# Optimization experiments

Measured on AMD Instinct MI355X. Metric: run time of the kernel, lower is better.

Reference implementation:

```python
import jax, jax.numpy as jnp
import numpy as np

N_ITEMS = 100000
N_EDGES = 800000
D = 64
N_LAYERS = 3  # config['ii_layers']


def setup_inputs() -> dict:
    key = jax.random.key(0)
    k1, k2, k3, k4 = jax.random.split(key, 4)
    rows = jax.random.randint(k1, (N_EDGES,), 0, N_ITEMS, dtype=jnp.int64 if jax.config.jax_enable_x64 else jnp.int32)
    cols = jax.random.randint(k2, (N_EDGES,), 0, N_ITEMS, dtype=jnp.int64 if jax.config.jax_enable_x64 else jnp.int32)
    vals = jax.random.uniform(k3, (N_EDGES,), dtype=jnp.float32)
    item_embeddings = jax.random.normal(k4, (N_ITEMS, D), dtype=jnp.float32)
    return {"rows": rows, "cols": cols, "vals": vals, "item_embeddings": item_embeddings}


def _spmm(rows, cols, vals, x):
    # sparse.mm(A, x) with A in COO: out[r] += vals[e] * x[c] for each edge e=(r,c)
    msgs = vals[:, None] * x[cols]            # [E, D] gathered & weighted messages
    return jax.ops.segment_sum(msgs, rows, num_segments=N_ITEMS)


def reference(rows, cols, vals, item_embeddings):
    # HyperConv: iterate SpMM, average initial + all layer outputs (fused running sum).
    acc = item_embeddings
    cur = item_embeddings
    for _ in range(N_LAYERS):
        cur = _spmm(rows, cols, vals, cur)
        acc = acc + cur
    return acc / jnp.asarray(N_LAYERS + 1, dtype=item_embeddings.dtype)
```

## Files before the change

### kernel.cpp

```cpp
#include <hip/hip_runtime.h>
#include <hip/hip_fp16.h>


#define NI 100000
#define NE 800000
#define DD 64

#define RPB  512
#define BINS ((NI + RPB - 1) / RPB)
#define EPB  4096
#define P1B  ((NE + EPB - 1) / EPB)
#define CAP  5120
#define BC   32

__global__ __launch_bounds__(256) void part1_k(const int* __restrict__ rows,
                                               const int* __restrict__ cols,
                                               const float* __restrict__ vals,
                                               int* __restrict__ bin_cnt,
                                               int2* __restrict__ binned) {
    __shared__ int hist[BINS], base[BINS], cur[BINS];
    int t = threadIdx.x;
    for (int i = t; i < BINS; i += 256) hist[i] = 0;
    __syncthreads();
    int e0 = blockIdx.x * EPB;
    for (int i = t; i < EPB; i += 256) {
        int e = e0 + i;
        if (e < NE) atomicAdd(&hist[rows[e] >> 9], 1);
    }
    __syncthreads();
    for (int i = t; i < BINS; i += 256) {
        int c = hist[i];
        base[i] = c ? atomicAdd(&bin_cnt[i], c) : 0;
        cur[i] = 0;
    }
    __syncthreads();
    for (int i = t; i < EPB; i += 256) {
        int e = e0 + i;
        if (e < NE) {
            int r = rows[e];
            int b = r >> 9;
            int pos = base[b] + atomicAdd(&cur[b], 1);
            if (pos < CAP)
                binned[(size_t)b * CAP + pos] =
                    make_int2(((r & 511) << 17) | cols[e], __float_as_int(vals[e]));
        }
    }
}

__global__ __launch_bounds__(256) void part2_k(const int* __restrict__ bin_cnt,
                                               const int2* __restrict__ binned,
                                               int2* __restrict__ bucket,
                                               int* __restrict__ fill) {
    __shared__ int cur[RPB];
    int t = threadIdx.x;
    int b = blockIdx.x;
    for (int i = t; i < RPB; i += 256) cur[i] = 0;
    __syncthreads();
    int cnt = bin_cnt[b];
    if (cnt > CAP) cnt = CAP;
    const int2* src = binned + (size_t)b * CAP;
    for (int i = t; i < cnt; i += 256) {
        int2 e = src[i];
        int rl = e.x >> 17;
        int pos = atomicAdd(&cur[rl], 1);
        if (pos < BC)
            bucket[((size_t)b * RPB + rl) * BC + pos] = make_int2(e.x & 0x1FFFF, e.y);
    }
    __syncthreads();
    for (int i = t; i < RPB; i += 256) {
        int r = b * RPB + i;
        if (r < NI) {
            int c = (cur[i] < BC) ? cur[i] : BC;
            if (c & 1) {
                bucket[((size_t)b * RPB + i) * BC + c] = make_int2(0, 0);
                c++;
            }
            fill[r] = c;
        }
    }
}

__global__ __launch_bounds__(256) void convert_k(const float4* __restrict__ x,
                                                 __half* __restrict__ xh, int n4) {
    int i = blockIdx.x * 256 + threadIdx.x;
    if (i < n4) {
        float4 v = x[i];
        __half2* dst = (__half2*)(xh + (size_t)i * 4);
        dst[0] = __floats2half2_rn(v.x, v.y);
        dst[1] = __floats2half2_rn(v.z, v.w);
    }
}

template <int MODE>
__global__ __launch_bounds__(256) void spmm_k(const int* __restrict__ fill,
                                              const int2* __restrict__ bucket,
                                              const __half* __restrict__ xin,
                                              __half* __restrict__ nxt,
                                              const float* __restrict__ x0,
                                              const __half* __restrict__ s1,
                                              float* __restrict__ outp) {
    int tid  = threadIdx.x;
    int lane = tid & 63;
    int grp  = lane >> 3;
    int ll   = lane & 7;
    int r    = blockIdx.x * 32 + (tid >> 6) * 8 + grp;
    int deg  = fill[r];
    const int2* ep = bucket + (size_t)r * BC;

    float a0 = 0.f, a1 = 0.f, a2 = 0.f, a3 = 0.f;
    float a4 = 0.f, a5 = 0.f, a6 = 0.f, a7 = 0.f;

    for (int j = 0; j < deg; j += 2) {
        int2 e0 = ep[j];
        int2 e1 = ep[j + 1];
        const uint4* p0 = (const uint4*)(xin + (size_t)e0.x * DD + 8 * ll);
        const uint4* p1 = (const uint4*)(xin + (size_t)e1.x * DD + 8 * ll);
        uint4 g0 = *p0;
        uint4 g1 = *p1;
        float v0 = __int_as_float(e0.y);
        float v1 = __int_as_float(e1.y);
        float2 f;
        f = __half22float2(*(__half2*)&g0.x); a0 += v0 * f.x; a1 += v0 * f.y;
        f = __half22float2(*(__half2*)&g0.y); a2 += v0 * f.x; a3 += v0 * f.y;
        f = __half22float2(*(__half2*)&g0.z); a4 += v0 * f.x; a5 += v0 * f.y;
        f = __half22float2(*(__half2*)&g0.w); a6 += v0 * f.x; a7 += v0 * f.y;
        f = __half22float2(*(__half2*)&g1.x); a0 += v1 * f.x; a1 += v1 * f.y;
        f = __half22float2(*(__half2*)&g1.y); a2 += v1 * f.x; a3 += v1 * f.y;
        f = __half22float2(*(__half2*)&g1.z); a4 += v1 * f.x; a5 += v1 * f.y;
        f = __half22float2(*(__half2*)&g1.w); a6 += v1 * f.x; a7 += v1 * f.y;
    }

    if (MODE == 2) {
        size_t fo = (size_t)r * DD + 8 * ll;
        const float4* xp = (const float4*)(x0 + fo);
        float4 xa = xp[0], xb = xp[1];
        uint4 s1u = *(const uint4*)(s1 + fo);
        uint4 s2u = *(const uint4*)(xin + fo);
        float4 oa, ob;
        float2 f1, f2;
        f1 = __half22float2(*(__half2*)&s1u.x); f2 = __half22float2(*(__half2*)&s2u.x);
        oa.x = (xa.x + f1.x + f2.x + a0) * 0.25f;
        oa.y = (xa.y + f1.y + f2.y + a1) * 0.25f;
        f1 = __half22float2(*(__half2*)&s1u.y); f2 = __half22float2(*(__half2*)&s2u.y);
        oa.z = (xa.z + f1.x + f2.x + a2) * 0.25f;
        oa.w = (xa.w + f1.y + f2.y + a3) * 0.25f;
        f1 = __half22float2(*(__half2*)&s1u.z); f2 = __half22float2(*(__half2*)&s2u.z);
        ob.x = (xb.x + f1.x + f2.x + a4) * 0.25f;
        ob.y = (xb.y + f1.y + f2.y + a5) * 0.25f;
        f1 = __half22float2(*(__half2*)&s1u.w); f2 = __half22float2(*(__half2*)&s2u.w);
        ob.z = (xb.z + f1.x + f2.x + a6) * 0.25f;
        ob.w = (xb.w + f1.y + f2.y + a7) * 0.25f;
        float4* op = (float4*)(outp + fo);
        op[0] = oa;
        op[1] = ob;
    } else {
        uint4 o;
        __half2 h;
        h = __floats2half2_rn(a0, a1); o.x = *(uint*)&h;
        h = __floats2half2_rn(a2, a3); o.y = *(uint*)&h;
        h = __floats2half2_rn(a4, a5); o.z = *(uint*)&h;
        h = __floats2half2_rn(a6, a7); o.w = *(uint*)&h;
        *(uint4*)(nxt + (size_t)r * DD + 8 * ll) = o;
    }
}

#define NB ((NI + 255) / 256)

__global__ __launch_bounds__(256) void init_k(const float4* __restrict__ x,
                                              float4* __restrict__ cur,
                                              float4* __restrict__ acc, int n4) {
    int i = blockIdx.x * 256 + threadIdx.x;
    if (i < n4) { float4 v = x[i]; cur[i] = v; acc[i] = v; }
}

__global__ __launch_bounds__(256) void hist_k(const int* __restrict__ rows,
                                              int* __restrict__ counts) {
    int e = blockIdx.x * 256 + threadIdx.x;
    if (e < NE) atomicAdd(&counts[rows[e]], 1);
}

__global__ __launch_bounds__(256) void scan1_k(const int* __restrict__ counts,
                                               int* __restrict__ bsum) {
    __shared__ int s[256];
    int t = threadIdx.x;
    int i = blockIdx.x * 256 + t;
    s[t] = (i < NI) ? counts[i] : 0;
    __syncthreads();
    for (int off = 128; off > 0; off >>= 1) {
        if (t < off) s[t] += s[t + off];
        __syncthreads();
    }
    if (t == 0) bsum[blockIdx.x] = s[0];
}

__global__ __launch_bounds__(512) void scan2_k(int* __restrict__ bsum) {
    __shared__ int s[512];
    int t = threadIdx.x;
    int v = (t < NB) ? bsum[t] : 0;
    s[t] = v;
    __syncthreads();
    for (int off = 1; off < 512; off <<= 1) {
        int tmp = (t >= off) ? s[t - off] : 0;
        __syncthreads();
        s[t] += tmp;
        __syncthreads();
    }
    if (t < NB) bsum[t] = s[t] - v;
}

__global__ __launch_bounds__(256) void scan3_k(const int* __restrict__ counts,
                                               const int* __restrict__ bsum,
                                               int* __restrict__ rowptr) {
    __shared__ int s[256];
    int t = threadIdx.x;
    int i = blockIdx.x * 256 + t;
    int v = (i < NI) ? counts[i] : 0;
    s[t] = v;
    __syncthreads();
    for (int off = 1; off < 256; off <<= 1) {
        int tmp = (t >= off) ? s[t - off] : 0;
        __syncthreads();
        s[t] += tmp;
        __syncthreads();
    }
    int excl = s[t] - v + bsum[blockIdx.x];
    if (i < NI) rowptr[i] = excl;
    if (i == NI - 1) rowptr[NI] = excl + v;
}

__global__ __launch_bounds__(256) void scatter_k(const int* __restrict__ rows,
                                                 const int* __restrict__ cols,
                                                 const float* __restrict__ vals,
                                                 const int* __restrict__ rowptr,
                                                 int* __restrict__ fillc,
                                                 int2* __restrict__ edges) {
    int e = blockIdx.x * 256 + threadIdx.x;
    if (e < NE) {
        int r = rows[e];
        int pos = rowptr[r] + atomicAdd(&fillc[r], 1);
        edges[pos] = make_int2(cols[e], __float_as_int(vals[e]));
    }
}

__global__ __launch_bounds__(256) void spmm_csr_k(const int* __restrict__ rowptr,
                                                  const int2* __restrict__ edges,
                                                  const float* __restrict__ x,
                                                  float* __restrict__ nxt,
                                                  float* __restrict__ acc,
                                                  int last) {
    int r = __builtin_amdgcn_readfirstlane(blockIdx.x * 4 + (threadIdx.x >> 6));
    int lane = threadIdx.x & 63;
    int beg = rowptr[r];
    int end = rowptr[r + 1];
    float s = 0.f;
    int j = beg;
    for (; j + 3 < end; j += 4) {
        int2 e0 = edges[j], e1 = edges[j + 1], e2 = edges[j + 2], e3 = edges[j + 3];
        float g0 = x[(size_t)e0.x * DD + lane];
        float g1 = x[(size_t)e1.x * DD + lane];
        float g2 = x[(size_t)e2.x * DD + lane];
        float g3 = x[(size_t)e3.x * DD + lane];
        s += __int_as_float(e0.y) * g0; s += __int_as_float(e1.y) * g1;
        s += __int_as_float(e2.y) * g2; s += __int_as_float(e3.y) * g3;
    }
    for (; j < end; ++j) {
        int2 e = edges[j];
        s += __int_as_float(e.y) * x[(size_t)e.x * DD + lane];
    }
    size_t o = (size_t)r * DD + lane;
    if (last) acc[o] = (acc[o] + s) * 0.25f;
    else { nxt[o] = s; acc[o] += s; }
}

extern "C" void kernel_launch(void* const* d_in, const int* in_sizes, int n_in,
                              void* d_out, int out_size, void* d_ws, size_t ws_size,
                              hipStream_t stream) {
    const int*   rows = (const int*)d_in[0];
    const int*   cols = (const int*)d_in[1];
    const float* vals = (const float*)d_in[2];
    const float* x    = (const float*)d_in[3];
    float* outp = (float*)d_out;

    const size_t fbuf  = (size_t)NI * DD * sizeof(float);
    const size_t hbuf  = (size_t)NI * DD * sizeof(__half);
    const int    n4        = NI * DD / 4;
    const int    grid_elem = (n4 + 255) / 256;

    char* wsp = (char*)d_ws;

    size_t off_xh     = 0;
    size_t off_s1     = off_xh + hbuf;
    size_t off_s2     = off_s1 + hbuf;
    size_t off_bucket = off_s2 + hbuf;
    size_t off_binned = off_bucket + (size_t)NI * BC * 8;
    size_t off_fill   = off_binned + (size_t)BINS * CAP * 8;
    size_t off_bcnt   = off_fill + (size_t)NI * 4;
    size_t need       = off_bcnt + (size_t)BINS * 4;

    if (ws_size >= need) {
        __half* xh      = (__half*)(wsp + off_xh);
        __half* s1h     = (__half*)(wsp + off_s1);
        __half* s2h     = (__half*)(wsp + off_s2);
        int2*   bucket  = (int2*)(wsp + off_bucket);
        int2*   binned  = (int2*)(wsp + off_binned);
        int*    fill    = (int*)(wsp + off_fill);
        int*    bin_cnt = (int*)(wsp + off_bcnt);

        hipMemsetAsync(bin_cnt, 0, BINS * sizeof(int), stream);
        part1_k<<<P1B, 256, 0, stream>>>(rows, cols, vals, bin_cnt, binned);
        part2_k<<<BINS, 256, 0, stream>>>(bin_cnt, binned, bucket, fill);
        convert_k<<<grid_elem, 256, 0, stream>>>((const float4*)x, xh, n4);

        const int grid_spmm = NI / 32;
        spmm_k<0><<<grid_spmm, 256, 0, stream>>>(fill, bucket, xh,  s1h, nullptr, nullptr, nullptr);
        spmm_k<1><<<grid_spmm, 256, 0, stream>>>(fill, bucket, s1h, s2h, nullptr, nullptr, nullptr);
        spmm_k<2><<<grid_spmm, 256, 0, stream>>>(fill, bucket, s2h, nullptr, x, s1h, outp);
        return;
    }

    const int grid_edge = (NE + 255) / 256;
    const int grid_csr  = NI / 4;

    float* bufA   = (float*)wsp;
    float* bufB   = (float*)(wsp + fbuf);
    int2*  edges  = (int2*)(wsp + 2 * fbuf);
    int*   rowptr = (int*)(wsp + 2 * fbuf + (size_t)NE * 8);
    int*   counts = rowptr + (NI + 1);
    int*   bsum   = counts + NI;

    hipMemsetAsync(counts, 0, NI * sizeof(int), stream);
    hist_k<<<grid_edge, 256, 0, stream>>>(rows, counts);
    scan1_k<<<NB, 256, 0, stream>>>(counts, bsum);
    scan2_k<<<1, 512, 0, stream>>>(bsum);
    scan3_k<<<NB, 256, 0, stream>>>(counts, bsum, rowptr);
    hipMemsetAsync(counts, 0, NI * sizeof(int), stream);
    scatter_k<<<grid_edge, 256, 0, stream>>>(rows, cols, vals, rowptr, counts, edges);
    init_k<<<grid_elem, 256, 0, stream>>>((const float4*)x, (float4*)bufA,
                                          (float4*)outp, n4);
    spmm_csr_k<<<grid_csr, 256, 0, stream>>>(rowptr, edges, bufA, bufB, outp, 0);
    spmm_csr_k<<<grid_csr, 256, 0, stream>>>(rowptr, edges, bufB, bufA, outp, 0);
    spmm_csr_k<<<grid_csr, 256, 0, stream>>>(rowptr, edges, bufA, bufB, outp, 1);
}
```

Measured before the change: 188.4 us.

## Replace capped per-row buckets with exact CSR and chunk-major feature layout

Measured after the change: 495.5 us. 163% more time.

```diff
diff --git a/kernel.cpp b/kernel.cpp
--- a/kernel.cpp
+++ b/kernel.cpp
@@ -5,13 +5,14 @@
 #define NI 100000
 #define NE 800000
 #define DD 64
+#define NCH 8
+#define CF  8
 
 #define RPB  512
 #define BINS ((NI + RPB - 1) / RPB)
-#define EPB  4096
+#define EPB  1024
 #define P1B  ((NE + EPB - 1) / EPB)
 #define CAP  5120
-#define BC   32
 
 __global__ __launch_bounds__(256) void part1_k(const int* __restrict__ rows,
                                                const int* __restrict__ cols,
@@ -49,93 +50,120 @@
 
 __global__ __launch_bounds__(256) void part2_k(const int* __restrict__ bin_cnt,
                                                const int2* __restrict__ binned,
-                                               int2* __restrict__ bucket,
-                                               int* __restrict__ fill) {
-    __shared__ int cur[RPB];
+                                               int2* __restrict__ edges,
+                                               int* __restrict__ rowptr) {
+    __shared__ int cur[RPB], off[RPB];
+    __shared__ long long ecache[CAP];
+    __shared__ int bb;
     int t = threadIdx.x;
     int b = blockIdx.x;
+
     for (int i = t; i < RPB; i += 256) cur[i] = 0;
-    __syncthreads();
-    int cnt = bin_cnt[b];
-    if (cnt > CAP) cnt = CAP;
+    if (t < BINS) off[t] = min(bin_cnt[t], CAP);
+    __syncthreads();
+    if (t == 0) {
+        int s = 0;
+        for (int i = 0; i < b; i++) s += off[i];
+        bb = s;
+    }
+    int cnt = min(bin_cnt[b], CAP);
     const int2* src = binned + (size_t)b * CAP;
+    __syncthreads();
     for (int i = t; i < cnt; i += 256) {
         int2 e = src[i];
-        int rl = e.x >> 17;
-        int pos = atomicAdd(&cur[rl], 1);
-        if (pos < BC)
-            bucket[((size_t)b * RPB + rl) * BC + pos] = make_int2(e.x & 0x1FFFF, e.y);
+        atomicAdd(&cur[e.x >> 17], 1);
+        ecache[i] = ((long long)e.y << 32) | (unsigned int)e.x;
+    }
+    __syncthreads();
+    if (t < 64) {
+        int base_i = t * 8;
+        int loc[8];
+        int s = 0;
+        #pragma unroll
+        for (int k = 0; k < 8; k++) { loc[k] = s; s += cur[base_i + k]; }
+        int excl = s;
+        #pragma unroll
+        for (int d = 1; d < 64; d <<= 1) {
+            int v = __shfl_up(excl, d, 64);
+            if (t >= d) excl += v;
+        }
+        excl -= s;
+        #pragma unroll
+        for (int k = 0; k < 8; k++) off[base_i + k] = excl + loc[k];
     }
     __syncthreads();
     for (int i = t; i < RPB; i += 256) {
         int r = b * RPB + i;
-        if (r < NI) {
-            int c = (cur[i] < BC) ? cur[i] : BC;
-            if (c & 1) {
-                bucket[((size_t)b * RPB + i) * BC + c] = make_int2(0, 0);
-                c++;
-            }
-            fill[r] = c;
-        }
-    }
-}
-
-__global__ __launch_bounds__(256) void convert_k(const float4* __restrict__ x,
-                                                 __half* __restrict__ xh, int n4) {
-    int i = blockIdx.x * 256 + threadIdx.x;
-    if (i < n4) {
-        float4 v = x[i];
-        __half2* dst = (__half2*)(xh + (size_t)i * 4);
-        dst[0] = __floats2half2_rn(v.x, v.y);
-        dst[1] = __floats2half2_rn(v.z, v.w);
+        if (r < NI) rowptr[r] = bb + off[i];
+        cur[i] = 0;
+    }
+    if (b == BINS - 1 && t == 0) rowptr[NI] = bb + cnt;
+    __syncthreads();
+    for (int i = t; i < cnt; i += 256) {
+        long long e = ecache[i];
+        int lo = (int)e;
+        int rl = (lo >> 17) & 511;
+        int pos = bb + off[rl] + atomicAdd(&cur[rl], 1);
+        edges[pos] = make_int2(lo & 0x1FFFF, (int)(e >> 32));
+    }
+}
+
+__global__ __launch_bounds__(256) void convert_k(const float* __restrict__ x,
+                                                 __half* __restrict__ xh) {
+    int r = blockIdx.x * 256 + threadIdx.x;
+    int c = blockIdx.y;
+    if (r < NI) {
+        const float4* xp = (const float4*)(x + (size_t)r * DD + c * CF);
+        float4 xa = xp[0], xb = xp[1];
+        uint4 o;
+        __half2 h;
+        h = __floats2half2_rn(xa.x, xa.y); o.x = *(unsigned int*)&h;
+        h = __floats2half2_rn(xa.z, xa.w); o.y = *(unsigned int*)&h;
+        h = __floats2half2_rn(xb.x, xb.y); o.z = *(unsigned int*)&h;
+        h = __floats2half2_rn(xb.w, xb.w); o.w = *(unsigned int*)&h;
+        h = __floats2half2_rn(xb.z, xb.w); o.w = *(unsigned int*)&h;
+        *(uint4*)(xh + (size_t)c * NI * CF + (size_t)r * CF) = o;
     }
 }
 
 template <int MODE>
-__global__ __launch_bounds__(256) void spmm_k(const int* __restrict__ fill,
-                                              const int2* __restrict__ bucket,
+__global__ __launch_bounds__(256) void spmm_k(const int* __restrict__ rowptr,
+                                              const long long* __restrict__ edges,
                                               const __half* __restrict__ xin,
                                               __half* __restrict__ nxt,
                                               const float* __restrict__ x0,
                                               const __half* __restrict__ s1,
                                               float* __restrict__ outp) {
-    int tid  = threadIdx.x;
-    int lane = tid & 63;
-    int grp  = lane >> 3;
-    int ll   = lane & 7;
-    int r    = blockIdx.x * 32 + (tid >> 6) * 8 + grp;
-    int deg  = fill[r];
-    const int2* ep = bucket + (size_t)r * BC;
+    int chunk  = blockIdx.x & 7;
+    int rowblk = blockIdx.x >> 3;
+    int r = rowblk * 256 + threadIdx.x;
+    bool act = (r < NI);
+    int beg = act ? rowptr[r] : 0;
+    int end = act ? rowptr[r + 1] : 0;
+    const __half* xc = xin + (size_t)chunk * NI * CF;
 
     float a0 = 0.f, a1 = 0.f, a2 = 0.f, a3 = 0.f;
     float a4 = 0.f, a5 = 0.f, a6 = 0.f, a7 = 0.f;
 
-    for (int j = 0; j < deg; j += 2) {
-        int2 e0 = ep[j];
-        int2 e1 = ep[j + 1];
-        const uint4* p0 = (const uint4*)(xin + (size_t)e0.x * DD + 8 * ll);
-        const uint4* p1 = (const uint4*)(xin + (size_t)e1.x * DD + 8 * ll);
-        uint4 g0 = *p0;
-        uint4 g1 = *p1;
-        float v0 = __int_as_float(e0.y);
-        float v1 = __int_as_float(e1.y);
+    for (int j = beg; j < end; ++j) {
+        long long e = __builtin_nontemporal_load(edges + j);
+        int col = (int)e;
+        float v = __int_as_float((int)(e >> 32));
+        uint4 g = *(const uint4*)(xc + (size_t)col * CF);
         float2 f;
-        f = __half22float2(*(__half2*)&g0.x); a0 += v0 * f.x; a1 += v0 * f.y;
-        f = __half22float2(*(__half2*)&g0.y); a2 += v0 * f.x; a3 += v0 * f.y;
-        f = __half22float2(*(__half2*)&g0.z); a4 += v0 * f.x; a5 += v0 * f.y;
-        f = __half22float2(*(__half2*)&g0.w); a6 += v0 * f.x; a7 += v0 * f.y;
-        f = __half22float2(*(__half2*)&g1.x); a0 += v1 * f.x; a1 += v1 * f.y;
-        f = __half22float2(*(__half2*)&g1.y); a2 += v1 * f.x; a3 += v1 * f.y;
-        f = __half22float2(*(__half2*)&g1.z); a4 += v1 * f.x; a5 += v1 * f.y;
-        f = __half22float2(*(__half2*)&g1.w); a6 += v1 * f.x; a7 += v1 * f.y;
-    }
-
+        f = __half22float2(*(__half2*)&g.x); a0 += v * f.x; a1 += v * f.y;
+        f = __half22float2(*(__half2*)&g.y); a2 += v * f.x; a3 += v * f.y;
+        f = __half22float2(*(__half2*)&g.z); a4 += v * f.x; a5 += v * f.y;
+        f = __half22float2(*(__half2*)&g.w); a6 += v * f.x; a7 += v * f.y;
+    }
+
+    if (!act) return;
+    size_t co = (size_t)chunk * NI * CF + (size_t)r * CF;
     if (MODE == 2) {
-        size_t fo = (size_t)r * DD + 8 * ll;
-        const float4* xp = (const float4*)(x0 + fo);
+        const float4* xp = (const float4*)(x0 + (size_t)r * DD + chunk * CF);
         float4 xa = xp[0], xb = xp[1];
-        uint4 s1u = *(const uint4*)(s1 + fo);
-        uint4 s2u = *(const uint4*)(xin + fo);
+        uint4 s1u = *(const uint4*)(s1 + co);
+        uint4 s2u = *(const uint4*)(xin + co);
         float4 oa, ob;
         float2 f1, f2;
         f1 = __half22float2(*(__half2*)&s1u.x); f2 = __half22float2(*(__half2*)&s2u.x);
@@ -150,17 +178,17 @@
         f1 = __half22float2(*(__half2*)&s1u.w); f2 = __half22float2(*(__half2*)&s2u.w);
         ob.z = (xb.z + f1.x + f2.x + a6) * 0.25f;
         ob.w = (xb.w + f1.y + f2.y + a7) * 0.25f;
-        float4* op = (float4*)(outp + fo);
+        float4* op = (float4*)(outp + (size_t)r * DD + chunk * CF);
         op[0] = oa;
         op[1] = ob;
     } else {
         uint4 o;
         __half2 h;
-        h = __floats2half2_rn(a0, a1); o.x = *(uint*)&h;
-        h = __floats2half2_rn(a2, a3); o.y = *(uint*)&h;
-        h = __floats2half2_rn(a4, a5); o.z = *(uint*)&h;
-        h = __floats2half2_rn(a6, a7); o.w = *(uint*)&h;
-        *(uint4*)(nxt + (size_t)r * DD + 8 * ll) = o;
+        h = __floats2half2_rn(a0, a1); o.x = *(unsigned int*)&h;
+        h = __floats2half2_rn(a2, a3); o.y = *(unsigned int*)&h;
+        h = __floats2half2_rn(a4, a5); o.z = *(unsigned int*)&h;
+        h = __floats2half2_rn(a6, a7); o.w = *(unsigned int*)&h;
+        *(uint4*)(nxt + co) = o;
     }
 }
 
@@ -281,49 +309,52 @@
     const float* x    = (const float*)d_in[3];
     float* outp = (float*)d_out;
 
-    const size_t fbuf  = (size_t)NI * DD * sizeof(float);
-    const size_t hbuf  = (size_t)NI * DD * sizeof(__half);
-    const int    n4        = NI * DD / 4;
-    const int    grid_elem = (n4 + 255) / 256;
+    const size_t fbuf = (size_t)NI * DD * sizeof(float);
+    const size_t hbuf = (size_t)NI * DD * sizeof(__half);
 
     char* wsp = (char*)d_ws;
 
     size_t off_xh     = 0;
     size_t off_s1     = off_xh + hbuf;
     size_t off_s2     = off_s1 + hbuf;
-    size_t off_bucket = off_s2 + hbuf;
-    size_t off_binned = off_bucket + (size_t)NI * BC * 8;
-    size_t off_fill   = off_binned + (size_t)BINS * CAP * 8;
-    size_t off_bcnt   = off_fill + (size_t)NI * 4;
+    size_t off_binned = off_s2 + hbuf;
+    size_t off_edges  = off_binned + (size_t)BINS * CAP * 8;
+    size_t off_rowptr = off_edges + (size_t)NE * 8;
+    size_t off_bcnt   = off_rowptr + ((size_t)NI + 2) * 4;
     size_t need       = off_bcnt + (size_t)BINS * 4;
 
     if (ws_size >= need) {
         __half* xh      = (__half*)(wsp + off_xh);
         __half* s1h     = (__half*)(wsp + off_s1);
         __half* s2h     = (__half*)(wsp + off_s2);
-        int2*   bucket  = (int2*)(wsp + off_bucket);
         int2*   binned  = (int2*)(wsp + off_binned);
-        int*    fill    = (int*)(wsp + off_fill);
+        int2*   edges   = (int2*)(wsp + off_edges);
+        int*    rowptr  = (int*)(wsp + off_rowptr);
         int*    bin_cnt = (int*)(wsp + off_bcnt);
 
         hipMemsetAsync(bin_cnt, 0, BINS * sizeof(int), stream);
         part1_k<<<P1B, 256, 0, stream>>>(rows, cols, vals, bin_cnt, binned);
-        part2_k<<<BINS, 256, 0, stream>>>(bin_cnt, binned, bucket, fill);
-        convert_k<<<grid_elem, 256, 0, stream>>>((const float4*)x, xh, n4);
-
-        const int grid_spmm = NI / 32;
-        spmm_k<0><<<grid_spmm, 256, 0, stream>>>(fill, bucket, xh,  s1h, nullptr, nullptr, nullptr);
-        spmm_k<1><<<grid_spmm, 256, 0, stream>>>(fill, bucket, s1h, s2h, nullptr, nullptr, nullptr);
-        spmm_k<2><<<grid_spmm, 256, 0, stream>>>(fill, bucket, s2h, nullptr, x, s1h, outp);
+        part2_k<<<BINS, 256, 0, stream>>>(bin_cnt, binned, edges, rowptr);
+        convert_k<<<dim3((NI + 255) / 256, NCH), 256, 0, stream>>>(x, xh);
+
+        const int grid_spmm = ((NI + 255) / 256) * NCH;
+        spmm_k<0><<<grid_spmm, 256, 0, stream>>>(rowptr, (const long long*)edges,
+                                                 xh, s1h, nullptr, nullptr, nullptr);
+        spmm_k<1><<<grid_spmm, 256, 0, stream>>>(rowptr, (const long long*)edges,
+                                                 s1h, s2h, nullptr, nullptr, nullptr);
+        spmm_k<2><<<grid_spmm, 256, 0, stream>>>(rowptr, (const long long*)edges,
+                                                 s2h, nullptr, x, s1h, outp);
         return;
     }
 
+    const int n4        = NI * DD / 4;
+    const int grid_elem = (n4 + 255) / 256;
     const int grid_edge = (NE + 255) / 256;
     const int grid_csr  = NI / 4;
 
     float* bufA   = (float*)wsp;
     float* bufB   = (float*)(wsp + fbuf);
-    int2*  edges  = (int2*)(wsp + 2 * fbuf);
+    int2*  edgesF = (int2*)(wsp + 2 * fbuf);
     int*   rowptr = (int*)(wsp + 2 * fbuf + (size_t)NE * 8);
     int*   counts = rowptr + (NI + 1);
     int*   bsum   = counts + NI;
@@ -334,10 +365,10 @@
     scan2_k<<<1, 512, 0, stream>>>(bsum);
     scan3_k<<<NB, 256, 0, stream>>>(counts, bsum, rowptr);
     hipMemsetAsync(counts, 0, NI * sizeof(int), stream);
-    scatter_k<<<grid_edge, 256, 0, stream>>>(rows, cols, vals, rowptr, counts, edges);
+    scatter_k<<<grid_edge, 256, 0, stream>>>(rows, cols, vals, rowptr, counts, edgesF);
     init_k<<<grid_elem, 256, 0, stream>>>((const float4*)x, (float4*)bufA,
                                           (float4*)outp, n4);
-    spmm_csr_k<<<grid_csr, 256, 0, stream>>>(rowptr, edges, bufA, bufB, outp, 0);
-    spmm_csr_k<<<grid_csr, 256, 0, stream>>>(rowptr, edges, bufB, bufA, outp, 0);
-    spmm_csr_k<<<grid_csr, 256, 0, stream>>>(rowptr, edges, bufA, bufB, outp, 1);
-}
+    spmm_csr_k<<<grid_csr, 256, 0, stream>>>(rowptr, edgesF, bufA, bufB, outp, 0);
+    spmm_csr_k<<<grid_csr, 256, 0, stream>>>(rowptr, edgesF, bufB, bufA, outp, 0);
+    spmm_csr_k<<<grid_csr, 256, 0, stream>>>(rowptr, edgesF, bufA, bufB, outp, 1);
+}
```
